# Optimization experiments

Hardware: AMD Instinct MI355X
Metric: run time of the kernel (lower is better)

The kernel has to match this reference:

```python
import jax, jax.numpy as jnp
import numpy as np

B, S, D = 4, 4096, 1024


def setup_inputs() -> dict:
    key = jax.random.key(0)
    ks = jax.random.split(key, 4)
    scale = 1.0 / np.sqrt(D)
    x = jax.random.normal(ks[0], (B, S, D), dtype=jnp.float32)
    Wg = jax.random.normal(ks[1], (D, D), dtype=jnp.float32) * scale
    Wv = jax.random.normal(ks[2], (D, D), dtype=jnp.float32) * scale
    Wd = jax.random.normal(ks[3], (D, D), dtype=jnp.float32) * scale
    bg = jnp.zeros((D,), dtype=jnp.float32)
    bv = jnp.zeros((D,), dtype=jnp.float32)
    bd = jnp.ones((D,), dtype=jnp.float32)  # decay_bias_init = 1.0
    return {"x": x, "Wg": Wg, "bg": bg, "Wv": Wv, "bv": bv, "Wd": Wd, "bd": bd}


def _scan_causal(x_scan, a):
    # h_t = a_t * h_{t-1} + x_t, scanned over time; x_scan, a: [B,S,D]
    def step(h, inp):
        a_t, x_t = inp
        h = a_t * h + x_t
        return h, h

    h0 = jnp.zeros(x_scan.shape[::2], dtype=x_scan.dtype)  # [B,D]
    xs = (jnp.swapaxes(a, 0, 1), jnp.swapaxes(x_scan, 0, 1))  # [S,B,D]
    _, out = jax.lax.scan(step, h0, xs)
    return jnp.swapaxes(out, 0, 1)  # back to [B,S,D]


def reference(x, Wg, bg, Wv, bv, Wd, bd):
    # nn.Linear: y = x @ W.T + b
    g = jnp.einsum('bsd,ed->bse', x, Wg) + bg
    v = jnp.einsum('bsd,ed->bse', x, Wv) + bv
    d = jnp.einsum('bsd,ed->bse', x, Wd) + bd
    x_scan = jax.nn.sigmoid(g) * jnp.tanh(v)
    a = 0.001 + 0.998 * jax.nn.sigmoid(d)
    return _scan_causal(x_scan, a)
```

## Files before the change

kernel.cpp:

```cpp
#include <hip/hip_runtime.h>
#include <cstddef>
#include <cstdint>


typedef _Float16 f16;
typedef f16 f16x8 __attribute__((ext_vector_type(8)));
typedef float f32x4 __attribute__((ext_vector_type(4)));

#define S_LEN 4096
#define D_DIM 1024
#define B_DIM 4
#define M_TOT (B_DIM * S_LEN)
#define N_TOT (3 * D_DIM)
#define K_TOT D_DIM

#define CLEN 16
#define CPB (S_LEN / CLEN)
#define NCHUNK (B_DIM * CPB)

#define SEG 16
#define NSEG (CPB / SEG)

__device__ __forceinline__ void cvt8(const float* s, f16* d) {
  f32x4 a = *(const f32x4*)s;
  f32x4 b = *(const f32x4*)(s + 4);
  f16x8 o;
  o[0] = (f16)a[0]; o[1] = (f16)a[1]; o[2] = (f16)a[2]; o[3] = (f16)a[3];
  o[4] = (f16)b[0]; o[5] = (f16)b[1]; o[6] = (f16)b[2]; o[7] = (f16)b[3];
  *(f16x8*)d = o;
}

__global__ void cvt_all_kernel(const float* __restrict__ x, const float* __restrict__ w0,
                               const float* __restrict__ w1, const float* __restrict__ w2,
                               f16* __restrict__ Ah, f16* __restrict__ Bh) {
  int i = (blockIdx.x * 256 + threadIdx.x) * 8;
  if (i < M_TOT * K_TOT) {
    cvt8(x + i, Ah + i);
  } else {
    int w = i - M_TOT * K_TOT;
    int row = w >> 10;
    int col = w & 1023;
    int srow = row / 3;
    int mat = row - srow * 3;
    const float* s = (mat == 0) ? w0 : (mat == 1) ? w1 : w2;
    cvt8(s + srow * 1024 + col, Bh + w);
  }
}

#define BM 256
#define BN 192
#define BK 64
#define RAWP 200
#define XSP 72

#define AS_OFF 0
#define BS_OFF 32768
#define ABUF 16384
#define BBUF 12288
#define SMEM_H 57344

__device__ __forceinline__ void gl_lds16(const void* g, void* l) {
  __builtin_amdgcn_global_load_lds((const __attribute__((address_space(1))) void*)g,
                                   (__attribute__((address_space(3))) void*)l, 16, 0, 0);
}

__device__ __forceinline__ void act(float g, float v, float d, f16& xh, f16& ah) {
  float sg = 1.f / (1.f + __expf(-g));
  float tv = 1.f - 2.f / (__expf(2.f * v) + 1.f);
  float sd = 1.f / (1.f + __expf(-d));
  xh = (f16)(sg * tv);
  ah = (f16)(0.001f + 0.998f * sd);
}

__global__ __launch_bounds__(512, 2) void gemm_fused_kernel(
    const f16* __restrict__ A, const f16* __restrict__ Bt,
    const float* __restrict__ bg, const float* __restrict__ bv,
    const float* __restrict__ bd,
    f16* __restrict__ xsA, f16* __restrict__ aA,
    float* __restrict__ P, float* __restrict__ H,
    float* __restrict__ SP, float* __restrict__ SH) {
  __shared__ __attribute__((aligned(16))) f16 smem[SMEM_H];
  const int tid = threadIdx.x;
  const int lane = tid & 63;
  const int wave = tid >> 6;

  const int wg = blockIdx.x;
  const int orig = (wg & 7) * 128 + (wg >> 3);
  const int bx = orig & 15;
  const int by = orig >> 4;
  const int m0 = by * BM;
  const int bn0 = bx * BN;

  const int d = tid & 63;
  const int cc = tid >> 6;
  const int gd = (bx << 6) + d;
  const float Bg = bg[gd], Bv = bv[gd], Bd_ = bd[gd];

  const int srow = tid >> 3;
  const int sslot = (tid & 7) ^ (srow & 7);
  const f16* aSrc = A + (size_t)(m0 + srow) * K_TOT + sslot * 8;
  const f16* bSrc = Bt + (size_t)(bn0 + srow) * K_TOT + sslot * 8;
  f16* aDst0 = smem + AS_OFF + tid * 8;
  f16* bDst0 = smem + BS_OFF + tid * 8;

  const int wm = (wave >> 1) * 64;
  const int wn = (wave & 1) * 96;
  const int lm = lane & 15;
  const int q = lane >> 4;
  const int sw0 = ((0 * 4 + q) ^ (lm & 7)) * 8;
  const int sw1 = ((1 * 4 + q) ^ (lm & 7)) * 8;

  f32x4 acc[4][6] = {};

  auto STAGE = [&](int tile, int buf) {
    const size_t k0 = (size_t)tile * BK;
#pragma unroll
    for (int r = 0; r < 4; ++r)
      gl_lds16(aSrc + (size_t)r * 64 * K_TOT + k0, aDst0 + buf * ABUF + r * 4096);
#pragma unroll
    for (int r = 0; r < 3; ++r)
      gl_lds16(bSrc + (size_t)r * 64 * K_TOT + k0, bDst0 + buf * BBUF + r * 4096);
  };

  STAGE(0, 0);
  STAGE(1, 1);

  for (int t = 0; t < 16; ++t) {
    if (t < 15) {
      asm volatile("s_waitcnt vmcnt(7)" ::: "memory");
    } else {
      asm volatile("s_waitcnt vmcnt(0)" ::: "memory");
    }
    __builtin_amdgcn_s_barrier();

    const f16* Acur = smem + AS_OFF + (t & 1) * ABUF;
    const f16* Bcur = smem + BS_OFF + (t & 1) * BBUF;
#pragma unroll
    for (int kk = 0; kk < 2; ++kk) {
      const int sw = kk ? sw1 : sw0;
      f16x8 af[4], bf[6];
#pragma unroll
      for (int i = 0; i < 4; ++i)
        af[i] = *(const f16x8*)&Acur[(wm + i * 16 + lm) * BK + sw];
#pragma unroll
      for (int j = 0; j < 6; ++j)
        bf[j] = *(const f16x8*)&Bcur[(wn + j * 16 + lm) * BK + sw];
#pragma unroll
      for (int i = 0; i < 4; ++i)
#pragma unroll
        for (int j = 0; j < 6; ++j)
          acc[i][j] = __builtin_amdgcn_mfma_f32_16x16x32_f16(af[i], bf[j], acc[i][j], 0, 0, 0);
    }

    if (t < 14) {
      __builtin_amdgcn_s_barrier();
      STAGE(t + 2, t & 1);
    }
  }
  __syncthreads();

  f16* Raw = smem;
  f16* xsL = smem + 25600;
  f16* aLs = smem + 34816;
  float* segP = (float*)(smem + 44032);
  float* segH = segP + 1024;

#pragma unroll
  for (int half = 0; half < 2; ++half) {
    if ((wave >> 2) == half) {
      const int r0 = ((wave >> 1) & 1) * 64 + ((lane >> 4) << 2);
      const int c0 = wn + (lane & 15);
#pragma unroll
      for (int i = 0; i < 4; ++i)
#pragma unroll
        for (int j = 0; j < 6; ++j)
#pragma unroll
          for (int r = 0; r < 4; ++r)
            Raw[(r0 + i * 16 + r) * RAWP + c0 + j * 16] = (f16)acc[i][j][r];
    }
    __syncthreads();

    {
      float p = 1.f, h = 0.f;
#pragma unroll
      for (int i = 0; i < CLEN; ++i) {
        const int r = cc * CLEN + i;
        const f16* t3 = &Raw[r * RAWP + 3 * d];
        f16 xh, ah;
        act((float)t3[0] + Bg, (float)t3[1] + Bv, (float)t3[2] + Bd_, xh, ah);
        xsL[r * XSP + d] = xh;
        aLs[r * XSP + d] = ah;
        float xf = (float)xh, af_ = (float)ah;
        h = af_ * h + xf;
        p *= af_;
      }
      const int gs = (m0 >> 4) + half * 8 + cc;
      P[(size_t)gs * D_DIM + gd] = p;
      H[(size_t)gs * D_DIM + gd] = h;
      segP[(half * 8 + cc) * 64 + d] = p;
      segH[(half * 8 + cc) * 64 + d] = h;
    }
    __syncthreads();

#pragma unroll
    for (int rr = 0; rr < 2; ++rr) {
      const int row = rr * 64 + (tid >> 3);
      const int col = (tid & 7) * 8;
      const size_t gi = (size_t)(m0 + half * 128 + row) * D_DIM + (bx << 6) + col;
      *(f16x8*)(xsA + gi) = *(const f16x8*)&xsL[row * XSP + col];
      *(f16x8*)(aA + gi) = *(const f16x8*)&aLs[row * XSP + col];
    }
    __syncthreads();
  }

  if (tid < 64) {
    float ps = 1.f, hs = 0.f;
#pragma unroll
    for (int s = 0; s < 16; ++s) {
      const float pp = segP[s * 64 + tid];
      const float hh = segH[s * 64 + tid];
      hs = pp * hs + hh;
      ps *= pp;
    }
    const size_t so = (size_t)by * D_DIM + (bx << 6) + tid;
    SP[so] = ps;
    SH[so] = hs;
  }
}

__global__ void scan3_kernel(const f16* __restrict__ xsA, const f16* __restrict__ aA,
                             const float* __restrict__ P, const float* __restrict__ Hc,
                             const float* __restrict__ SP, const float* __restrict__ SH,
                             float* __restrict__ out) {
  const int u = blockIdx.x * 256 + threadIdx.x;
  const int cg = u & 127;
  const int b = (u >> 7) & 3;
  const int ck = u >> 9;
  const int s = ck >> 4;
  const int ch = cg * 8;

  float h[8];
#pragma unroll
  for (int j = 0; j < 8; ++j) h[j] = 0.f;

  for (int s2 = 0; s2 < s; ++s2) {
    const size_t off = (size_t)(b * NSEG + s2) * D_DIM + ch;
    f32x4 sp0 = *(const f32x4*)(SP + off);
    f32x4 sp1 = *(const f32x4*)(SP + off + 4);
    f32x4 sh0 = *(const f32x4*)(SH + off);
    f32x4 sh1 = *(const f32x4*)(SH + off + 4);
#pragma unroll
    for (int j = 0; j < 4; ++j) h[j] = sp0[j] * h[j] + sh0[j];
#pragma unroll
    for (int j = 0; j < 4; ++j) h[4 + j] = sp1[j] * h[4 + j] + sh1[j];
  }
  for (int c = s * SEG; c < ck; ++c) {
    const size_t off = (size_t)(b * CPB + c) * D_DIM + ch;
    f32x4 p0 = *(const f32x4*)(P + off);
    f32x4 p1 = *(const f32x4*)(P + off + 4);
    f32x4 h0 = *(const f32x4*)(Hc + off);
    f32x4 h1 = *(const f32x4*)(Hc + off + 4);
#pragma unroll
    for (int j = 0; j < 4; ++j) h[j] = p0[j] * h[j] + h0[j];
#pragma unroll
    for (int j = 0; j < 4; ++j) h[4 + j] = p1[j] * h[4 + j] + h1[j];
  }

  const int t0 = ck * CLEN;
#pragma unroll 4
  for (int t = t0; t < t0 + CLEN; ++t) {
    const size_t m = (size_t)b * S_LEN + t;
    f16x8 xs8 = *(const f16x8*)(xsA + m * D_DIM + ch);
    f16x8 a8 = *(const f16x8*)(aA + m * D_DIM + ch);
#pragma unroll
    for (int j = 0; j < 8; ++j) h[j] = (float)a8[j] * h[j] + (float)xs8[j];
    float* op = out + m * D_DIM + ch;
    *(f32x4*)op = *(f32x4*)h;
    *(f32x4*)(op + 4) = *(f32x4*)(h + 4);
  }
}

extern "C" void kernel_launch(void* const* d_in, const int* in_sizes, int n_in,
                              void* d_out, int out_size, void* d_ws, size_t ws_size,
                              hipStream_t stream) {
  const float* x = (const float*)d_in[0];
  const float* Wg = (const float*)d_in[1];
  const float* bg = (const float*)d_in[2];
  const float* Wv = (const float*)d_in[3];
  const float* bv = (const float*)d_in[4];
  const float* Wd = (const float*)d_in[5];
  const float* bd = (const float*)d_in[6];
  float* out = (float*)d_out;

  char* ws = (char*)d_ws;
  f16* Ah = (f16*)(ws);
  f16* Bh = (f16*)(ws + 33554432);
  f16* xsA = (f16*)(ws + 39845888);
  f16* aA = (f16*)(ws + 73400320);
  float* P = (float*)(ws + 106954752);
  float* H = (float*)(ws + 111149056);
  float* SP = (float*)(ws + 115343360);
  float* SH = (float*)(ws + 115605504);

  cvt_all_kernel<<<9728, 256, 0, stream>>>(x, Wg, Wv, Wd, Ah, Bh);
  gemm_fused_kernel<<<1024, 512, 0, stream>>>(Ah, Bh, bg, bv, bd, xsA, aA, P, H, SP, SH);
  scan3_kernel<<<512, 256, 0, stream>>>(xsA, aA, P, H, SP, SH, out);
}
```

Baseline: 285.3 us.

## Halve GEMM K-tile and LDS footprint to fit four blocks per CU

```diff
diff --git a/kernel.cpp b/kernel.cpp
--- a/kernel.cpp
+++ b/kernel.cpp
@@ -49,15 +49,15 @@
 
 #define BM 256
 #define BN 192
-#define BK 64
+#define BK 32
 #define RAWP 200
 #define XSP 72
 
 #define AS_OFF 0
-#define BS_OFF 32768
-#define ABUF 16384
-#define BBUF 12288
-#define SMEM_H 57344
+#define BS_OFF 16384
+#define ABUF 8192
+#define BBUF 6144
+#define SMEM_H 28672
 
 __device__ __forceinline__ void gl_lds16(const void* g, void* l) {
   __builtin_amdgcn_global_load_lds((const __attribute__((address_space(1))) void*)g,
@@ -72,7 +72,7 @@
   ah = (f16)(0.001f + 0.998f * sd);
 }
 
-__global__ __launch_bounds__(512, 2) void gemm_fused_kernel(
+__global__ __launch_bounds__(512, 4) void gemm_fused_kernel(
     const f16* __restrict__ A, const f16* __restrict__ Bt,
     const float* __restrict__ bg, const float* __restrict__ bv,
     const float* __restrict__ bd,
@@ -92,42 +92,44 @@
   const int bn0 = bx * BN;
 
   const int d = tid & 63;
-  const int cc = tid >> 6;
   const int gd = (bx << 6) + d;
   const float Bg = bg[gd], Bv = bv[gd], Bd_ = bd[gd];
 
-  const int srow = tid >> 3;
-  const int sslot = (tid & 7) ^ (srow & 7);
+  const int tau = tid & 255;
+  const int srow = tau >> 2;
+  const int sslot = (tau & 3) ^ ((tau >> 3) & 3);
   const f16* aSrc = A + (size_t)(m0 + srow) * K_TOT + sslot * 8;
   const f16* bSrc = Bt + (size_t)(bn0 + srow) * K_TOT + sslot * 8;
-  f16* aDst0 = smem + AS_OFF + tid * 8;
-  f16* bDst0 = smem + BS_OFF + tid * 8;
+  f16* aDst0 = smem + AS_OFF + tau * 8;
+  f16* bDst0 = smem + BS_OFF + tau * 8;
 
   const int wm = (wave >> 1) * 64;
   const int wn = (wave & 1) * 96;
   const int lm = lane & 15;
-  const int q = lane >> 4;
-  const int sw0 = ((0 * 4 + q) ^ (lm & 7)) * 8;
-  const int sw1 = ((1 * 4 + q) ^ (lm & 7)) * 8;
+  const int kswz = (((lane >> 4) ^ ((lm >> 1) & 3)) << 3);
 
   f32x4 acc[4][6] = {};
 
   auto STAGE = [&](int tile, int buf) {
     const size_t k0 = (size_t)tile * BK;
-#pragma unroll
-    for (int r = 0; r < 4; ++r)
-      gl_lds16(aSrc + (size_t)r * 64 * K_TOT + k0, aDst0 + buf * ABUF + r * 4096);
-#pragma unroll
-    for (int r = 0; r < 3; ++r)
-      gl_lds16(bSrc + (size_t)r * 64 * K_TOT + k0, bDst0 + buf * BBUF + r * 4096);
+    if (wave < 4) {
+#pragma unroll
+      for (int r = 0; r < 4; ++r)
+        gl_lds16(aSrc + (size_t)r * 64 * K_TOT + k0, aDst0 + buf * ABUF + r * 2048);
+    } else {
+#pragma unroll
+      for (int r = 0; r < 3; ++r)
+        gl_lds16(bSrc + (size_t)r * 64 * K_TOT + k0, bDst0 + buf * BBUF + r * 2048);
+    }
   };
 
   STAGE(0, 0);
   STAGE(1, 1);
 
-  for (int t = 0; t < 16; ++t) {
-    if (t < 15) {
-      asm volatile("s_waitcnt vmcnt(7)" ::: "memory");
+  for (int t = 0; t < 32; ++t) {
+    if (t < 31) {
+      if (wave < 4) asm volatile("s_waitcnt vmcnt(4)" ::: "memory");
+      else          asm volatile("s_waitcnt vmcnt(3)" ::: "memory");
     } else {
       asm volatile("s_waitcnt vmcnt(0)" ::: "memory");
     }
@@ -135,24 +137,20 @@
 
     const f16* Acur = smem + AS_OFF + (t & 1) * ABUF;
     const f16* Bcur = smem + BS_OFF + (t & 1) * BBUF;
-#pragma unroll
-    for (int kk = 0; kk < 2; ++kk) {
-      const int sw = kk ? sw1 : sw0;
-      f16x8 af[4], bf[6];
-#pragma unroll
-      for (int i = 0; i < 4; ++i)
-        af[i] = *(const f16x8*)&Acur[(wm + i * 16 + lm) * BK + sw];
+    f16x8 af[4], bf[6];
+#pragma unroll
+    for (int i = 0; i < 4; ++i)
+      af[i] = *(const f16x8*)&Acur[(wm + i * 16 + lm) * BK + kswz];
+#pragma unroll
+    for (int j = 0; j < 6; ++j)
+      bf[j] = *(const f16x8*)&Bcur[(wn + j * 16 + lm) * BK + kswz];
+#pragma unroll
+    for (int i = 0; i < 4; ++i)
 #pragma unroll
       for (int j = 0; j < 6; ++j)
-        bf[j] = *(const f16x8*)&Bcur[(wn + j * 16 + lm) * BK + sw];
-#pragma unroll
-      for (int i = 0; i < 4; ++i)
-#pragma unroll
-        for (int j = 0; j < 6; ++j)
-          acc[i][j] = __builtin_amdgcn_mfma_f32_16x16x32_f16(af[i], bf[j], acc[i][j], 0, 0, 0);
-    }
-
-    if (t < 14) {
+        acc[i][j] = __builtin_amdgcn_mfma_f32_16x16x32_f16(af[i], bf[j], acc[i][j], 0, 0, 0);
+
+    if (t < 30) {
       __builtin_amdgcn_s_barrier();
       STAGE(t + 2, t & 1);
     }
@@ -160,16 +158,17 @@
   __syncthreads();
 
   f16* Raw = smem;
-  f16* xsL = smem + 25600;
-  f16* aLs = smem + 34816;
-  float* segP = (float*)(smem + 44032);
+  f16* xsL = smem + 12800;
+  f16* aLs = smem + 17408;
+  float* segP = (float*)(smem + 22016);
   float* segH = segP + 1024;
-
-#pragma unroll
-  for (int half = 0; half < 2; ++half) {
-    if ((wave >> 2) == half) {
-      const int r0 = ((wave >> 1) & 1) * 64 + ((lane >> 4) << 2);
-      const int c0 = wn + (lane & 15);
+  const int cc = (tid >> 6) & 3;
+
+#pragma unroll
+  for (int qq = 0; qq < 4; ++qq) {
+    if ((wave >> 1) == qq) {
+      const int r0 = (lane >> 4) << 2;
+      const int c0 = wn + lm;
 #pragma unroll
       for (int i = 0; i < 4; ++i)
 #pragma unroll
@@ -180,7 +179,7 @@
     }
     __syncthreads();
 
-    {
+    if (tid < 256) {
       float p = 1.f, h = 0.f;
 #pragma unroll
       for (int i = 0; i < CLEN; ++i) {
@@ -194,19 +193,18 @@
         h = af_ * h + xf;
         p *= af_;
       }
-      const int gs = (m0 >> 4) + half * 8 + cc;
+      const int gs = (m0 >> 4) + qq * 4 + cc;
       P[(size_t)gs * D_DIM + gd] = p;
       H[(size_t)gs * D_DIM + gd] = h;
-      segP[(half * 8 + cc) * 64 + d] = p;
-      segH[(half * 8 + cc) * 64 + d] = h;
+      segP[(qq * 4 + cc) * 64 + d] = p;
+      segH[(qq * 4 + cc) * 64 + d] = h;
     }
     __syncthreads();
 
-#pragma unroll
-    for (int rr = 0; rr < 2; ++rr) {
-      const int row = rr * 64 + (tid >> 3);
+    {
+      const int row = tid >> 3;
       const int col = (tid & 7) * 8;
-      const size_t gi = (size_t)(m0 + half * 128 + row) * D_DIM + (bx << 6) + col;
+      const size_t gi = (size_t)(m0 + qq * 64 + row) * D_DIM + (bx << 6) + col;
       *(f16x8*)(xsA + gi) = *(const f16x8*)&xsL[row * XSP + col];
       *(f16x8*)(aA + gi) = *(const f16x8*)&aLs[row * XSP + col];
     }
```

New measurement: 358.3 us. +25.6%, slower.

## Fuse x fp32-to-fp16 conversion into GEMM A-tile staging

Applied to the files above, without the earlier changes.

```diff
diff --git a/kernel.cpp b/kernel.cpp
--- a/kernel.cpp
+++ b/kernel.cpp
@@ -30,21 +30,15 @@
   *(f16x8*)d = o;
 }
 
-__global__ void cvt_all_kernel(const float* __restrict__ x, const float* __restrict__ w0,
-                               const float* __restrict__ w1, const float* __restrict__ w2,
-                               f16* __restrict__ Ah, f16* __restrict__ Bh) {
-  int i = (blockIdx.x * 256 + threadIdx.x) * 8;
-  if (i < M_TOT * K_TOT) {
-    cvt8(x + i, Ah + i);
-  } else {
-    int w = i - M_TOT * K_TOT;
-    int row = w >> 10;
-    int col = w & 1023;
-    int srow = row / 3;
-    int mat = row - srow * 3;
-    const float* s = (mat == 0) ? w0 : (mat == 1) ? w1 : w2;
-    cvt8(s + srow * 1024 + col, Bh + w);
-  }
+__global__ void cvt_w_kernel(const float* __restrict__ w0, const float* __restrict__ w1,
+                             const float* __restrict__ w2, f16* __restrict__ Bh) {
+  int w = (blockIdx.x * 256 + threadIdx.x) * 8;
+  int row = w >> 10;
+  int col = w & 1023;
+  int srow = row / 3;
+  int mat = row - srow * 3;
+  const float* s = (mat == 0) ? w0 : (mat == 1) ? w1 : w2;
+  cvt8(s + srow * 1024 + col, Bh + w);
 }
 
 #define BM 256
@@ -73,7 +67,7 @@
 }
 
 __global__ __launch_bounds__(512, 2) void gemm_fused_kernel(
-    const f16* __restrict__ A, const f16* __restrict__ Bt,
+    const float* __restrict__ X, const f16* __restrict__ Bt,
     const float* __restrict__ bg, const float* __restrict__ bv,
     const float* __restrict__ bd,
     f16* __restrict__ xsA, f16* __restrict__ aA,
@@ -92,16 +86,16 @@
   const int bn0 = bx * BN;
 
   const int d = tid & 63;
-  const int cc = tid >> 6;
+  const int cc = (tid >> 6) & 3;
   const int gd = (bx << 6) + d;
   const float Bg = bg[gd], Bv = bv[gd], Bd_ = bd[gd];
 
   const int srow = tid >> 3;
   const int sslot = (tid & 7) ^ (srow & 7);
-  const f16* aSrc = A + (size_t)(m0 + srow) * K_TOT + sslot * 8;
+  const float* xA = X + (size_t)(m0 + srow) * K_TOT + (tid & 7) * 8;
   const f16* bSrc = Bt + (size_t)(bn0 + srow) * K_TOT + sslot * 8;
-  f16* aDst0 = smem + AS_OFF + tid * 8;
   f16* bDst0 = smem + BS_OFF + tid * 8;
+  f16* aDstW = smem + AS_OFF + srow * 64 + sslot * 8;
 
   const int wm = (wave >> 1) * 64;
   const int wn = (wave & 1) * 96;
@@ -111,65 +105,81 @@
   const int sw1 = ((1 * 4 + q) ^ (lm & 7)) * 8;
 
   f32x4 acc[4][6] = {};
-
-  auto STAGE = [&](int tile, int buf) {
+  f32x4 ar[8];
+
+  auto stageA_load = [&](int tile) {
     const size_t k0 = (size_t)tile * BK;
 #pragma unroll
-    for (int r = 0; r < 4; ++r)
-      gl_lds16(aSrc + (size_t)r * 64 * K_TOT + k0, aDst0 + buf * ABUF + r * 4096);
+    for (int r = 0; r < 4; ++r) {
+      const float* p = xA + (size_t)r * 64 * K_TOT + k0;
+      ar[2 * r] = *(const f32x4*)p;
+      ar[2 * r + 1] = *(const f32x4*)(p + 4);
+    }
+  };
+  auto stageA_write = [&](int buf) {
+#pragma unroll
+    for (int r = 0; r < 4; ++r) {
+      f16x8 o;
+#pragma unroll
+      for (int j = 0; j < 4; ++j) {
+        o[j] = (f16)ar[2 * r][j];
+        o[4 + j] = (f16)ar[2 * r + 1][j];
+      }
+      *(f16x8*)(aDstW + buf * ABUF + r * 4096) = o;
+    }
+  };
+  auto stageB = [&](int tile, int buf) {
+    const size_t k0 = (size_t)tile * BK;
 #pragma unroll
     for (int r = 0; r < 3; ++r)
       gl_lds16(bSrc + (size_t)r * 64 * K_TOT + k0, bDst0 + buf * BBUF + r * 4096);
   };
 
-  STAGE(0, 0);
-  STAGE(1, 1);
+  stageA_load(0);
+  stageB(0, 0);
+  stageA_write(0);
+  __syncthreads();
 
   for (int t = 0; t < 16; ++t) {
-    if (t < 15) {
-      asm volatile("s_waitcnt vmcnt(7)" ::: "memory");
-    } else {
-      asm volatile("s_waitcnt vmcnt(0)" ::: "memory");
-    }
-    __builtin_amdgcn_s_barrier();
-
-    const f16* Acur = smem + AS_OFF + (t & 1) * ABUF;
-    const f16* Bcur = smem + BS_OFF + (t & 1) * BBUF;
+    const int cur = t & 1, nxt = cur ^ 1;
+    const bool st = t < 15;
+    if (st) {
+      stageA_load(t + 1);
+      stageB(t + 1, nxt);
+    }
+    const f16* Ac = smem + AS_OFF + cur * ABUF;
+    const f16* Bc = smem + BS_OFF + cur * BBUF;
 #pragma unroll
     for (int kk = 0; kk < 2; ++kk) {
       const int sw = kk ? sw1 : sw0;
       f16x8 af[4], bf[6];
 #pragma unroll
       for (int i = 0; i < 4; ++i)
-        af[i] = *(const f16x8*)&Acur[(wm + i * 16 + lm) * BK + sw];
+        af[i] = *(const f16x8*)&Ac[(wm + i * 16 + lm) * BK + sw];
 #pragma unroll
       for (int j = 0; j < 6; ++j)
-        bf[j] = *(const f16x8*)&Bcur[(wn + j * 16 + lm) * BK + sw];
+        bf[j] = *(const f16x8*)&Bc[(wn + j * 16 + lm) * BK + sw];
 #pragma unroll
       for (int i = 0; i < 4; ++i)
 #pragma unroll
         for (int j = 0; j < 6; ++j)
           acc[i][j] = __builtin_amdgcn_mfma_f32_16x16x32_f16(af[i], bf[j], acc[i][j], 0, 0, 0);
     }
-
-    if (t < 14) {
-      __builtin_amdgcn_s_barrier();
-      STAGE(t + 2, t & 1);
-    }
-  }
-  __syncthreads();
+    if (st) stageA_write(nxt);
+    __syncthreads();
+  }
 
   f16* Raw = smem;
-  f16* xsL = smem + 25600;
-  f16* aLs = smem + 34816;
-  float* segP = (float*)(smem + 44032);
+  f16* xsL = smem + 12800;
+  f16* aLs = smem + 17408;
+  float* segP = (float*)(smem + 22016);
   float* segH = segP + 1024;
 
 #pragma unroll
-  for (int half = 0; half < 2; ++half) {
-    if ((wave >> 2) == half) {
-      const int r0 = ((wave >> 1) & 1) * 64 + ((lane >> 4) << 2);
-      const int c0 = wn + (lane & 15);
+  for (int qq = 0; qq < 4; ++qq) {
+    if ((wave >> 1) == qq) {
+      const int r0 = (lane >> 4) << 2;
+      const int c0 = wn + lm;
 #pragma unroll
       for (int i = 0; i < 4; ++i)
 #pragma unroll
@@ -180,7 +190,7 @@
     }
     __syncthreads();
 
-    {
+    if (tid < 256) {
       float p = 1.f, h = 0.f;
 #pragma unroll
       for (int i = 0; i < CLEN; ++i) {
@@ -194,19 +204,18 @@
         h = af_ * h + xf;
         p *= af_;
       }
-      const int gs = (m0 >> 4) + half * 8 + cc;
+      const int gs = (m0 >> 4) + qq * 4 + cc;
       P[(size_t)gs * D_DIM + gd] = p;
       H[(size_t)gs * D_DIM + gd] = h;
-      segP[(half * 8 + cc) * 64 + d] = p;
-      segH[(half * 8 + cc) * 64 + d] = h;
+      segP[(qq * 4 + cc) * 64 + d] = p;
+      segH[(qq * 4 + cc) * 64 + d] = h;
     }
     __syncthreads();
 
-#pragma unroll
-    for (int rr = 0; rr < 2; ++rr) {
-      const int row = rr * 64 + (tid >> 3);
+    {
+      const int row = tid >> 3;
       const int col = (tid & 7) * 8;
-      const size_t gi = (size_t)(m0 + half * 128 + row) * D_DIM + (bx << 6) + col;
+      const size_t gi = (size_t)(m0 + qq * 64 + row) * D_DIM + (bx << 6) + col;
       *(f16x8*)(xsA + gi) = *(const f16x8*)&xsL[row * XSP + col];
       *(f16x8*)(aA + gi) = *(const f16x8*)&aLs[row * XSP + col];
     }
@@ -293,16 +302,15 @@
   float* out = (float*)d_out;
 
   char* ws = (char*)d_ws;
-  f16* Ah = (f16*)(ws);
-  f16* Bh = (f16*)(ws + 33554432);
-  f16* xsA = (f16*)(ws + 39845888);
-  f16* aA = (f16*)(ws + 73400320);
-  float* P = (float*)(ws + 106954752);
-  float* H = (float*)(ws + 111149056);
-  float* SP = (float*)(ws + 115343360);
-  float* SH = (float*)(ws + 115605504);
-
-  cvt_all_kernel<<<9728, 256, 0, stream>>>(x, Wg, Wv, Wd, Ah, Bh);
-  gemm_fused_kernel<<<1024, 512, 0, stream>>>(Ah, Bh, bg, bv, bd, xsA, aA, P, H, SP, SH);
+  f16* Bh = (f16*)(ws);
+  f16* xsA = (f16*)(ws + 6291456);
+  f16* aA = (f16*)(ws + 39845888);
+  float* P = (float*)(ws + 73400320);
+  float* H = (float*)(ws + 77594624);
+  float* SP = (float*)(ws + 81788928);
+  float* SH = (float*)(ws + 82051072);
+
+  cvt_w_kernel<<<1536, 256, 0, stream>>>(Wg, Wv, Wd, Bh);
+  gemm_fused_kernel<<<1024, 512, 0, stream>>>(x, Bh, bg, bv, bd, xsA, aA, P, H, SP, SH);
   scan3_kernel<<<512, 256, 0, stream>>>(xsA, aA, P, H, SP, SH, out);
 }
```

After: 339.6 us. +19.0%, slower.
